# Kernel tuning notes

Measured on AMD Instinct MI355X. Metric: run time of the kernel, lower is better.

Reference implementation:

```python
import jax, jax.numpy as jnp
import numpy as np


def rotate_half(x):
    x1, x2 = jnp.split(x, 2, axis=-1)
    return jnp.concatenate([-x2, x1], axis=-1)


def setup_inputs() -> dict:
    key = jax.random.key(0)
    ks = jax.random.split(key, 7)
    B, L, D = 2, 2048, 2048
    H, KVH = 16, 4
    HD = D // H  # 128
    s = 0.02
    x = jax.random.normal(ks[0], (B, L, D), jnp.float32)
    # rotary tables: use realistic cos/sin of angles
    inv_freq = 1.0 / (10000.0 ** (np.arange(0, HD, 2, dtype=np.float32) / HD))
    t = np.arange(L, dtype=np.float32)
    freqs = np.outer(t, inv_freq)  # [L, HD/2]
    emb = np.concatenate([freqs, freqs], axis=-1)  # [L, HD]
    cos = jnp.asarray(np.cos(emb), jnp.float32)
    sin = jnp.asarray(np.sin(emb), jnp.float32)
    wq = jax.random.normal(ks[1], (D, H * HD), jnp.float32) * s
    wk = jax.random.normal(ks[2], (D, KVH * HD), jnp.float32) * s
    wv = jax.random.normal(ks[3], (D, KVH * HD), jnp.float32) * s
    wo = jax.random.normal(ks[4], (H * HD, D), jnp.float32) * s
    return {"x": x, "cos": cos, "sin": sin, "wq": wq, "wk": wk, "wv": wv, "wo": wo}


def reference(x, cos, sin, wq, wk, wv, wo):
    B, L, D = x.shape
    H, KVH = 16, 4
    HD = D // H
    n_rep = H // KVH
    q = (x @ wq).reshape(B, L, H, HD).transpose(0, 2, 1, 3)     # [B,H,L,hd]
    k = (x @ wk).reshape(B, L, KVH, HD).transpose(0, 2, 1, 3)   # [B,KVH,L,hd]
    v = (x @ wv).reshape(B, L, KVH, HD).transpose(0, 2, 1, 3)
    c = cos[None, None]  # [1,1,L,hd]
    s = sin[None, None]
    q = q * c + rotate_half(q) * s
    k = k * c + rotate_half(k) * s
    if n_rep > 1:
        k = jnp.repeat(k, n_rep, axis=1)
        v = jnp.repeat(v, n_rep, axis=1)
    scale = HD ** -0.5
    attn = jnp.einsum('bhqd,bhkd->bhqk', q, k) * scale  # [B,H,L,L]
    mask = jnp.triu(jnp.ones((L, L), bool), k=1)
    attn = jnp.where(mask, -jnp.inf, attn)
    attn = jax.nn.softmax(attn, axis=-1)
    out = jnp.einsum('bhqk,bhkd->bhqd', attn, v)
    out = out.transpose(0, 2, 1, 3).reshape(B, L, H * HD)
    return out @ wo
```

## Files before the change

kernel.cpp:

```cpp
#include <hip/hip_runtime.h>

typedef __attribute__((ext_vector_type(4))) float f32x4;
typedef __attribute__((ext_vector_type(8))) short s16x8;

__device__ __forceinline__ float bf2f(short b) {
  unsigned int u = ((unsigned int)(unsigned short)b) << 16;
  return __builtin_bit_cast(float, u);
}
__device__ __forceinline__ short f2bf(float f) {
  unsigned int u = __builtin_bit_cast(unsigned int, f);
  u = (u + 0x7fffu + ((u >> 16) & 1u)) >> 16;
  return (short)u;
}

__device__ __forceinline__ void async_copy16(void* lds, const void* g) {
  __builtin_amdgcn_global_load_lds((const __attribute__((address_space(1))) unsigned int*)g,
                                   (__attribute__((address_space(3))) unsigned int*)lds,
                                   16, 0, 0);
}


__global__ __launch_bounds__(256) void cvt_f32_bf16(const float* __restrict__ src,
                                                    short* __restrict__ dst, int n) {
  const int i = (blockIdx.x * 256 + threadIdx.x) * 4;
  if (i >= n) return;
  const float4 v = *(const float4*)&src[i];
  short4 o;
  o.x = f2bf(v.x); o.y = f2bf(v.y); o.z = f2bf(v.z); o.w = f2bf(v.w);
  *(short4*)&dst[i] = o;
}

__global__ __launch_bounds__(256) void transpose_cvt(const float* __restrict__ src,
                                                     short* __restrict__ dst, int R, int C) {
  __shared__ float t[32][33];
  const int c0 = blockIdx.x * 32, r0 = blockIdx.y * 32;
  const int tx = threadIdx.x & 31;
  const int ty = threadIdx.x >> 5;
#pragma unroll
  for (int i = 0; i < 4; ++i)
    t[ty + 8 * i][tx] = src[(size_t)(r0 + ty + 8 * i) * C + c0 + tx];
  __syncthreads();
#pragma unroll
  for (int i = 0; i < 4; ++i)
    dst[(size_t)(c0 + ty + 8 * i) * R + r0 + tx] = f2bf(t[tx][ty + 8 * i]);
}

__global__ __launch_bounds__(256) void transpose_v(const short* __restrict__ qkv,
                                                   short* __restrict__ vt) {
  __shared__ short t[32][33];
  const int l0 = blockIdx.x * 32;
  const int c0 = blockIdx.y * 32;
  const int b = blockIdx.z;
  const int tx = threadIdx.x & 31, ty = threadIdx.x >> 5;
#pragma unroll
  for (int i = 0; i < 4; ++i)
    t[ty + 8 * i][tx] = qkv[(size_t)(b * 2048 + l0 + ty + 8 * i) * 3072 + 2560 + c0 + tx];
  __syncthreads();
#pragma unroll
  for (int i = 0; i < 4; ++i) {
    const int c = c0 + ty + 8 * i;
    const int l = l0 + tx;
    const int kv = l & 63;
    const int kvp = (((kv & 15) * 4 + (kv >> 4)) ^ ((c & 7) << 3));
    vt[((size_t)b * 512 + c) * 2048 + (l & ~63) + kvp] = t[tx][ty + 8 * i];
  }
}


template <bool OUT_BF16>
__global__ __launch_bounds__(256) void gemm_bt(const short* __restrict__ A,
                                               const short* __restrict__ BT,
                                               void* __restrict__ Cout,
                                               int M, int N, int K) {
  __shared__ short As[128 * 32];
  __shared__ short Bs[128 * 32];
  const int tid = threadIdx.x;
  const int l = tid & 63, wid = tid >> 6;
  const int m0 = blockIdx.x * 128, n0 = blockIdx.y * 128;
  const int wr = (wid >> 1) * 64, wc = (wid & 1) * 64;
  const int lr = l & 15, lc = l >> 4;
  f32x4 acc[4][4] = {};

  for (int k0 = 0; k0 < K; k0 += 32) {
    __syncthreads();
#pragma unroll
    for (int i = 0; i < 2; ++i) {
      const int c = tid + 256 * i;
      const int row = c >> 2, kc = (c & 3) * 8;
      async_copy16((char*)As + (size_t)(i * 256 + wid * 64) * 16,
                   A + (size_t)(m0 + row) * K + k0 + kc);
      async_copy16((char*)Bs + (size_t)(i * 256 + wid * 64) * 16,
                   BT + (size_t)(n0 + row) * K + k0 + kc);
    }
    __syncthreads();
    s16x8 a[4], b[4];
#pragma unroll
    for (int m = 0; m < 4; ++m)
      a[m] = *(const s16x8*)&As[(wr + m * 16 + lr) * 32 + lc * 8];
#pragma unroll
    for (int n = 0; n < 4; ++n)
      b[n] = *(const s16x8*)&Bs[(wc + n * 16 + lr) * 32 + lc * 8];
#pragma unroll
    for (int m = 0; m < 4; ++m)
#pragma unroll
      for (int n = 0; n < 4; ++n)
        acc[m][n] = __builtin_amdgcn_mfma_f32_16x16x32_bf16(a[m], b[n], acc[m][n], 0, 0, 0);
  }

#pragma unroll
  for (int m = 0; m < 4; ++m)
#pragma unroll
    for (int n = 0; n < 4; ++n)
#pragma unroll
      for (int r = 0; r < 4; ++r) {
        const size_t row = (size_t)(m0 + wr + m * 16 + lc * 4 + r);
        const int col = n0 + wc + n * 16 + lr;
        if constexpr (OUT_BF16)
          ((short*)Cout)[row * N + col] = f2bf(acc[m][n][r]);
        else
          ((float*)Cout)[row * N + col] = acc[m][n][r];
      }
}


__global__ __launch_bounds__(256) void rope_kernel(short* __restrict__ qkv,
                                                   short* __restrict__ kswz,
                                                   const float* __restrict__ cosb,
                                                   const float* __restrict__ sinb) {
  const int idx = blockIdx.x * 256 + threadIdx.x;
  const int d = idx & 63;
  const int hh = (idx >> 6) % 20;
  const int row = idx / (64 * 20);
  const int lpos = row & 2047;
  const int col = (hh < 16) ? hh * 128 + d : 2048 + (hh - 16) * 128 + d;
  short* p = qkv + (size_t)row * 3072 + col;
  const float x1 = bf2f(p[0]);
  const float x2 = bf2f(p[64]);
  const float c = cosb[lpos * 128 + d];
  const float sn = sinb[lpos * 128 + d];
  const short o1 = f2bf(x1 * c - x2 * sn);
  const short o2 = f2bf(x2 * c + x1 * sn);
  if (hh < 16) {
    p[0] = o1;
    p[64] = o2;
  } else {
    const int b = row >> 11;
    const int kvh = hh - 16;
    short* kp = kswz + (((size_t)(b * 4 + kvh) * 2048) + lpos) * 128;
    const int sw = (lpos & 7) << 3;
    kp[d ^ sw] = o1;
    kp[(d + 64) ^ sw] = o2;
  }
}


__global__ __launch_bounds__(256) void flash_attn(const short* __restrict__ qkv,
                                                  const short* __restrict__ kswz,
                                                  const short* __restrict__ vt,
                                                  short* __restrict__ attn_out) {
  __shared__ short Ks[64 * 128];
  __shared__ short Vs[128 * 64];
  __shared__ short Pb[4][16 * 72];
  const int tid = threadIdx.x;
  const int l = tid & 63, w = tid >> 6;
  const int lr = l & 15, lc = l >> 4;
  const int sw = (lr & 7) << 3;
  const int qpair = blockIdx.x, h = blockIdx.y, b = blockIdx.z;
  const int kvh = h >> 2;
  const short* Qg = qkv + (size_t)b * 2048 * 3072 + h * 128;
  const short* Kg = kswz + ((size_t)(b * 4 + kvh) * 2048) * 128;
  const short* Vtg = vt + ((size_t)b * 512 + kvh * 128) * 2048;
  const float SCALE2 = 0.12751744166306968f;

#pragma unroll 1
  for (int seg = 0; seg < 2; ++seg) {
    const int qt = seg ? (31 - qpair) : qpair;
    const int qbase = qt * 64 + w * 16;

    s16x8 qf[4];
#pragma unroll
    for (int dc = 0; dc < 4; ++dc) {
      qf[dc] = *(const s16x8*)&Qg[(size_t)(qbase + lr) * 3072 + dc * 32 + lc * 8];
#pragma unroll
      for (int j = 0; j < 8; ++j) qf[dc][j] = f2bf(bf2f(qf[dc][j]) * SCALE2);
    }

    f32x4 oacc[8] = {};
    float mrow[4], ssum[4];
#pragma unroll
    for (int r = 0; r < 4; ++r) { mrow[r] = -__builtin_inff(); ssum[r] = 0.f; }
    const int nkt = qt + 1;

    for (int kt = 0; kt < nkt; ++kt) {
      const int kv0 = kt * 64;
      __syncthreads();
#pragma unroll
      for (int i = 0; i < 4; ++i) {
        async_copy16((char*)Ks + i * 4096 + w * 1024,
                     Kg + (size_t)kv0 * 128 + i * 2048 + w * 512 + l * 8);
        async_copy16((char*)Vs + i * 4096 + w * 1024,
                     Vtg + (size_t)(i * 32 + w * 8 + (l >> 3)) * 2048 + kv0 + (l & 7) * 8);
      }
      __syncthreads();

      f32x4 sacc[4] = {};
      __builtin_amdgcn_s_setprio(1);
#pragma unroll
      for (int cb = 0; cb < 4; ++cb)
#pragma unroll
        for (int dc = 0; dc < 4; ++dc) {
          const s16x8 kf = *(const s16x8*)&Ks[(cb * 16 + lr) * 128 + ((dc * 32 + lc * 8) ^ sw)];
          sacc[cb] = __builtin_amdgcn_mfma_f32_16x16x32_bf16(qf[dc], kf, sacc[cb], 0, 0, 0);
        }
      __builtin_amdgcn_s_setprio(0);

      const bool need_mask = (kt == qt);
#pragma unroll
      for (int r = 0; r < 4; ++r) {
        float s0 = sacc[0][r];
        float s1 = sacc[1][r];
        float s2 = sacc[2][r];
        float s3 = sacc[3][r];
        if (need_mask) {
          const int qrow = qbase + lc * 4 + r;
          if (kv0 + lr > qrow) s0 = -1e30f;
          if (kv0 + 16 + lr > qrow) s1 = -1e30f;
          if (kv0 + 32 + lr > qrow) s2 = -1e30f;
          if (kv0 + 48 + lr > qrow) s3 = -1e30f;
        }
        float rm = fmaxf(fmaxf(s0, s1), fmaxf(s2, s3));
        rm = fmaxf(rm, __shfl_xor(rm, 1, 64));
        rm = fmaxf(rm, __shfl_xor(rm, 2, 64));
        rm = fmaxf(rm, __shfl_xor(rm, 4, 64));
        rm = fmaxf(rm, __shfl_xor(rm, 8, 64));
        if (!__all(rm <= mrow[r] + 8.f)) {
          const float mnew = fmaxf(mrow[r], rm);
          const float resc = exp2f(mrow[r] - mnew);
          mrow[r] = mnew;
          ssum[r] *= resc;
#pragma unroll
          for (int db = 0; db < 8; ++db) oacc[db][r] *= resc;
        }
        const float m = mrow[r];
        const float p0 = exp2f(s0 - m);
        const float p1 = exp2f(s1 - m);
        const float p2 = exp2f(s2 - m);
        const float p3 = exp2f(s3 - m);
        float rs = (p0 + p1) + (p2 + p3);
        rs += __shfl_xor(rs, 1, 64);
        rs += __shfl_xor(rs, 2, 64);
        rs += __shfl_xor(rs, 4, 64);
        rs += __shfl_xor(rs, 8, 64);
        ssum[r] += rs;
        uint2 u;
        u.x = (unsigned)(unsigned short)f2bf(p0) | ((unsigned)(unsigned short)f2bf(p1) << 16);
        u.y = (unsigned)(unsigned short)f2bf(p2) | ((unsigned)(unsigned short)f2bf(p3) << 16);
        *(uint2*)&Pb[w][(lc * 4 + r) * 72 + lr * 4] = u;
      }

      __builtin_amdgcn_s_setprio(1);
#pragma unroll
      for (int kk = 0; kk < 2; ++kk) {
        const s16x8 pf = *(const s16x8*)&Pb[w][lr * 72 + kk * 32 + lc * 8];
#pragma unroll
        for (int db = 0; db < 8; ++db) {
          const s16x8 vf = *(const s16x8*)&Vs[(db * 16 + lr) * 64 + ((kk * 32 + lc * 8) ^ sw)];
          oacc[db] = __builtin_amdgcn_mfma_f32_16x16x32_bf16(pf, vf, oacc[db], 0, 0, 0);
        }
      }
      __builtin_amdgcn_s_setprio(0);
    }

#pragma unroll
    for (int r = 0; r < 4; ++r) {
      const float inv = 1.0f / ssum[r];
      const size_t orow = (size_t)b * 2048 + qbase + lc * 4 + r;
#pragma unroll
      for (int db = 0; db < 8; ++db)
        attn_out[orow * 2048 + h * 128 + db * 16 + lr] = f2bf(oacc[db][r] * inv);
    }
  }
}


extern "C" void kernel_launch(void* const* d_in, const int* in_sizes, int n_in,
                              void* d_out, int out_size, void* d_ws, size_t ws_size,
                              hipStream_t stream) {
  const float* x    = (const float*)d_in[0];
  const float* cosb = (const float*)d_in[1];
  const float* sinb = (const float*)d_in[2];
  const float* wq   = (const float*)d_in[3];
  const float* wk   = (const float*)d_in[4];
  const float* wv   = (const float*)d_in[5];
  const float* wo   = (const float*)d_in[6];
  float* out = (float*)d_out;

  char* ws = (char*)d_ws;
  short* xb    = (short*)(ws);
  short* vtb   = (short*)(ws);
  short* kswzb = (short*)(ws + 4194304);
  short* wqkvT = (short*)(ws + 16777216);
  short* woT   = (short*)(ws + 29360128);
  short* qkvb  = (short*)(ws + 37748736);
  short* attnb = (short*)(ws + 62914560);

  cvt_f32_bf16<<<8192, 256, 0, stream>>>(x, xb, 8388608);
  transpose_cvt<<<dim3(64, 64), 256, 0, stream>>>(wq, wqkvT, 2048, 2048);
  transpose_cvt<<<dim3(16, 64), 256, 0, stream>>>(wk, wqkvT + 2048 * 2048, 2048, 512);
  transpose_cvt<<<dim3(16, 64), 256, 0, stream>>>(wv, wqkvT + 2560 * 2048, 2048, 512);
  transpose_cvt<<<dim3(64, 64), 256, 0, stream>>>(wo, woT, 2048, 2048);

  gemm_bt<true><<<dim3(32, 24), 256, 0, stream>>>(xb, wqkvT, qkvb, 4096, 3072, 2048);
  rope_kernel<<<20480, 256, 0, stream>>>(qkvb, kswzb, cosb, sinb);
  transpose_v<<<dim3(64, 16, 2), 256, 0, stream>>>(qkvb, vtb);
  flash_attn<<<dim3(16, 16, 2), 256, 0, stream>>>(qkvb, kswzb, vtb, attnb);
  gemm_bt<false><<<dim3(32, 16), 256, 0, stream>>>(attnb, woT, out, 4096, 2048, 2048);
}
```

Before: 368.3 us.

## Transpose S MFMA so each lane owns one query row; row-sum via MFMA

Swaps the MFMA operand order for QK^T so each lane holds scores for a single query row across 16 keys. Row max then needs only two cross-lane shuffles instead of four per row, and the running max becomes a single scalar per lane. The softmax denominator is now accumulated with an extra MFMA against a ones vector, which removes the per-row shuffle reductions. P is packed with the hardware v_cvt_pk_bf16 instruction and written into a swizzled LDS layout, and the V-transpose permutation is simplified to match the new key order.

Result: faster. 334.5 us (-9.2%).

```diff
diff --git a/kernel.cpp b/kernel.cpp
--- a/kernel.cpp
+++ b/kernel.cpp
@@ -11,6 +11,11 @@
   unsigned int u = __builtin_bit_cast(unsigned int, f);
   u = (u + 0x7fffu + ((u >> 16) & 1u)) >> 16;
   return (short)u;
+}
+__device__ __forceinline__ unsigned cvt_pk_bf16(float a, float b) {
+  unsigned r;
+  asm("v_cvt_pk_bf16_f32 %0, %1, %2" : "=v"(r) : "v"(a), "v"(b));
+  return r;
 }
 
 __device__ __forceinline__ void async_copy16(void* lds, const void* g) {
@@ -60,8 +65,7 @@
   for (int i = 0; i < 4; ++i) {
     const int c = c0 + ty + 8 * i;
     const int l = l0 + tx;
-    const int kv = l & 63;
-    const int kvp = (((kv & 15) * 4 + (kv >> 4)) ^ ((c & 7) << 3));
+    const int kvp = (l & 63) ^ ((c & 7) << 3);
     vt[((size_t)b * 512 + c) * 2048 + (l & ~63) + kvp] = t[tx][ty + 8 * i];
   }
 }
@@ -160,7 +164,7 @@
                                                   short* __restrict__ attn_out) {
   __shared__ short Ks[64 * 128];
   __shared__ short Vs[128 * 64];
-  __shared__ short Pb[4][16 * 72];
+  __shared__ uint2 Pb[4][16][16];
   const int tid = threadIdx.x;
   const int l = tid & 63, w = tid >> 6;
   const int lr = l & 15, lc = l >> 4;
@@ -171,6 +175,9 @@
   const short* Kg = kswz + ((size_t)(b * 4 + kvh) * 2048) * 128;
   const short* Vtg = vt + ((size_t)b * 512 + kvh * 128) * 2048;
   const float SCALE2 = 0.12751744166306968f;
+  s16x8 ones;
+#pragma unroll
+  for (int j = 0; j < 8; ++j) ones[j] = (short)0x3F80;
 
 #pragma unroll 1
   for (int seg = 0; seg < 2; ++seg) {
@@ -186,9 +193,8 @@
     }
 
     f32x4 oacc[8] = {};
-    float mrow[4], ssum[4];
-#pragma unroll
-    for (int r = 0; r < 4; ++r) { mrow[r] = -__builtin_inff(); ssum[r] = 0.f; }
+    f32x4 osum = {0.f, 0.f, 0.f, 0.f};
+    float mrow = -__builtin_inff();
     const int nkt = qt + 1;
 
     for (int kt = 0; kt < nkt; ++kt) {
@@ -210,70 +216,74 @@
 #pragma unroll
         for (int dc = 0; dc < 4; ++dc) {
           const s16x8 kf = *(const s16x8*)&Ks[(cb * 16 + lr) * 128 + ((dc * 32 + lc * 8) ^ sw)];
-          sacc[cb] = __builtin_amdgcn_mfma_f32_16x16x32_bf16(qf[dc], kf, sacc[cb], 0, 0, 0);
+          sacc[cb] = __builtin_amdgcn_mfma_f32_16x16x32_bf16(kf, qf[dc], sacc[cb], 0, 0, 0);
         }
       __builtin_amdgcn_s_setprio(0);
 
-      const bool need_mask = (kt == qt);
-#pragma unroll
-      for (int r = 0; r < 4; ++r) {
-        float s0 = sacc[0][r];
-        float s1 = sacc[1][r];
-        float s2 = sacc[2][r];
-        float s3 = sacc[3][r];
-        if (need_mask) {
-          const int qrow = qbase + lc * 4 + r;
-          if (kv0 + lr > qrow) s0 = -1e30f;
-          if (kv0 + 16 + lr > qrow) s1 = -1e30f;
-          if (kv0 + 32 + lr > qrow) s2 = -1e30f;
-          if (kv0 + 48 + lr > qrow) s3 = -1e30f;
+      if (kt == qt) {
+        const int qrow = qbase + lr;
+#pragma unroll
+        for (int cb = 0; cb < 4; ++cb)
+#pragma unroll
+          for (int r = 0; r < 4; ++r)
+            if (kv0 + cb * 16 + lc * 4 + r > qrow) sacc[cb][r] = -1e30f;
+      }
+
+      float rm = sacc[0][0];
+#pragma unroll
+      for (int cb = 0; cb < 4; ++cb)
+#pragma unroll
+        for (int r = 0; r < 4; ++r)
+          if (cb | r) rm = fmaxf(rm, sacc[cb][r]);
+      rm = fmaxf(rm, __shfl_xor(rm, 16, 64));
+      rm = fmaxf(rm, __shfl_xor(rm, 32, 64));
+
+      if (!__all(rm <= mrow + 8.f)) {
+        const float mnew = fmaxf(mrow, rm);
+        const float resc = exp2f(mrow - mnew);
+        mrow = mnew;
+#pragma unroll
+        for (int r = 0; r < 4; ++r) {
+          const float rr = __shfl(resc, (l & 48) | (((l >> 4) & 3) * 4 + r), 64);
+          osum[r] *= rr;
+#pragma unroll
+          for (int db = 0; db < 8; ++db) oacc[db][r] *= rr;
         }
-        float rm = fmaxf(fmaxf(s0, s1), fmaxf(s2, s3));
-        rm = fmaxf(rm, __shfl_xor(rm, 1, 64));
-        rm = fmaxf(rm, __shfl_xor(rm, 2, 64));
-        rm = fmaxf(rm, __shfl_xor(rm, 4, 64));
-        rm = fmaxf(rm, __shfl_xor(rm, 8, 64));
-        if (!__all(rm <= mrow[r] + 8.f)) {
-          const float mnew = fmaxf(mrow[r], rm);
-          const float resc = exp2f(mrow[r] - mnew);
-          mrow[r] = mnew;
-          ssum[r] *= resc;
-#pragma unroll
-          for (int db = 0; db < 8; ++db) oacc[db][r] *= resc;
-        }
-        const float m = mrow[r];
-        const float p0 = exp2f(s0 - m);
-        const float p1 = exp2f(s1 - m);
-        const float p2 = exp2f(s2 - m);
-        const float p3 = exp2f(s3 - m);
-        float rs = (p0 + p1) + (p2 + p3);
-        rs += __shfl_xor(rs, 1, 64);
-        rs += __shfl_xor(rs, 2, 64);
-        rs += __shfl_xor(rs, 4, 64);
-        rs += __shfl_xor(rs, 8, 64);
-        ssum[r] += rs;
+      }
+
+#pragma unroll
+      for (int cb = 0; cb < 4; ++cb) {
+        const float p0 = exp2f(sacc[cb][0] - mrow);
+        const float p1 = exp2f(sacc[cb][1] - mrow);
+        const float p2 = exp2f(sacc[cb][2] - mrow);
+        const float p3 = exp2f(sacc[cb][3] - mrow);
         uint2 u;
-        u.x = (unsigned)(unsigned short)f2bf(p0) | ((unsigned)(unsigned short)f2bf(p1) << 16);
-        u.y = (unsigned)(unsigned short)f2bf(p2) | ((unsigned)(unsigned short)f2bf(p3) << 16);
-        *(uint2*)&Pb[w][(lc * 4 + r) * 72 + lr * 4] = u;
+        u.x = cvt_pk_bf16(p0, p1);
+        u.y = cvt_pk_bf16(p2, p3);
+        Pb[w][lr][(4 * cb + lc) ^ (lr & 7)] = u;
       }
 
       __builtin_amdgcn_s_setprio(1);
 #pragma unroll
       for (int kk = 0; kk < 2; ++kk) {
-        const s16x8 pf = *(const s16x8*)&Pb[w][lr * 72 + kk * 32 + lc * 8];
+        const uint2 plo = Pb[w][lr][(8 * kk + 2 * lc) ^ (lr & 7)];
+        const uint2 phi = Pb[w][lr][(8 * kk + 2 * lc + 1) ^ (lr & 7)];
+        union { uint2 u2[2]; s16x8 v; } pu;
+        pu.u2[0] = plo; pu.u2[1] = phi;
+        const s16x8 pf = pu.v;
 #pragma unroll
         for (int db = 0; db < 8; ++db) {
           const s16x8 vf = *(const s16x8*)&Vs[(db * 16 + lr) * 64 + ((kk * 32 + lc * 8) ^ sw)];
           oacc[db] = __builtin_amdgcn_mfma_f32_16x16x32_bf16(pf, vf, oacc[db], 0, 0, 0);
         }
+        osum = __builtin_amdgcn_mfma_f32_16x16x32_bf16(pf, ones, osum, 0, 0, 0);
       }
       __builtin_amdgcn_s_setprio(0);
     }
 
 #pragma unroll
     for (int r = 0; r < 4; ++r) {
-      const float inv = 1.0f / ssum[r];
+      const float inv = 1.0f / osum[r];
       const size_t orow = (size_t)b * 2048 + qbase + lc * 4 + r;
 #pragma unroll
       for (int db = 0; db < 8; ++db)
```
